# Kernel tuning notes

Measured on AMD Instinct MI355X. Metric: run time of the kernel, lower is better.

The kernel has to match this reference:

```python
import jax, jax.numpy as jnp
import numpy as np

B, T, V, H, E, MAX_OOV = 128, 200, 50257, 256, 128, 50


def setup_inputs() -> dict:
    key = jax.random.key(0)
    ks = jax.random.split(key, 17)
    s = 0.05  # param scale
    return {
        "decoder_input": jax.random.randint(ks[0], (B, 1), 0, V),
        "encoder_outputs": jax.random.normal(ks[1], (B, T, 2 * H), jnp.float32),
        "encoder_idxs": jax.random.randint(ks[2], (B, T), 0, V),
        "prev_state": jax.random.normal(ks[3], (1, B, H), jnp.float32),
        "selective_read": jax.random.normal(ks[4], (B, 1, 2 * H), jnp.float32) * s,
        "step": 1,
        "emb": jax.random.normal(ks[5], (V, E), jnp.float32) * s,
        "W_ih": jax.random.normal(ks[6], (3 * H, E + 2 * H), jnp.float32) * s,
        "W_hh": jax.random.normal(ks[7], (3 * H, H), jnp.float32) * s,
        "b_ih": jax.random.normal(ks[8], (3 * H,), jnp.float32) * s,
        "b_hh": jax.random.normal(ks[9], (3 * H,), jnp.float32) * s,
        "Wi_w": jax.random.normal(ks[10], (H, 2 * H), jnp.float32) * s,
        "Wi_b": jax.random.normal(ks[11], (H,), jnp.float32) * s,
        "Wg_w": jax.random.normal(ks[12], (V, H), jnp.float32) * s,
        "Wg_b": jax.random.normal(ks[13], (V,), jnp.float32) * s,
        "Wc_w": jax.random.normal(ks[14], (H, 2 * H), jnp.float32) * s,
        "Wc_b": jax.random.normal(ks[15], (H,), jnp.float32) * s,
    }


def _gru_cell(x, h, W_ih, W_hh, b_ih, b_hh):
    # torch GRUCell math, gate order r,z,n
    gi = x @ W_ih.T + b_ih
    gh = h @ W_hh.T + b_hh
    i_r, i_z, i_n = jnp.split(gi, 3, axis=-1)
    h_r, h_z, h_n = jnp.split(gh, 3, axis=-1)
    r = jax.nn.sigmoid(i_r + h_r)
    z = jax.nn.sigmoid(i_z + h_z)
    n = jnp.tanh(i_n + r * h_n)
    return (1.0 - z) * n + z * h


def reference(decoder_input, encoder_outputs, encoder_idxs, prev_state, selective_read,
              step, emb, W_ih, W_hh, b_ih, b_hh, Wi_w, Wi_b, Wg_w, Wg_b, Wc_w, Wc_b):
    dtype = encoder_outputs.dtype
    if step == 0:
        prev_state = (encoder_outputs[:, -1] @ Wi_w.T + Wi_b)[None]      # 1,B,H
        selective_read = jnp.zeros((B, 1, 2 * H), dtype)
    embedded = emb[decoder_input[:, 0]]                                   # B,E
    gru_in = jnp.concatenate([selective_read[:, 0], embedded], axis=-1)   # B,2H+E
    decode_hidden = _gru_cell(gru_in, prev_state[0], W_ih, W_hh, b_ih, b_hh)  # B,H

    score_g = decode_hidden @ Wg_w.T + Wg_b                               # B,V
    enc_proj = jnp.tanh(jnp.einsum('bte,he->bth', encoder_outputs, Wc_w) + Wc_b)  # B,T,H
    score_c = jnp.tanh(jnp.einsum('bth,bh->bt', enc_proj, decode_hidden))         # B,T
    score_c = score_c + jnp.where(encoder_idxs == 0, -10000.0, 0.0).astype(dtype)

    probs = jax.nn.softmax(jnp.concatenate([score_g, score_c], axis=1), axis=1)   # B,V+T
    prob_g, prob_c = probs[:, :V], probs[:, V:]
    prob_g = jnp.concatenate([prob_g, jnp.full((B, MAX_OOV), 1e-4, dtype)], axis=1)  # B,V+oov

    # copy-distribution aggregation: scatter-add prob_c by vocab id (replaces one-hot bmm)
    prob_c_to_g = jnp.zeros((B, V + MAX_OOV), dtype).at[
        jnp.arange(B)[:, None], encoder_idxs].add(prob_c)
    prob_out = (prob_c_to_g + prob_g)[:, None, :]                          # B,1,V+oov

    # selective read for next step
    match = (encoder_idxs == decoder_input).astype(dtype)                  # B,T
    tot = match.sum(axis=1, keepdims=True)
    match = jnp.where(tot > 1, match / tot, match)
    prob_appeared = prob_c * match
    selective_read_new = jnp.einsum('bt,bte->be', prob_appeared, encoder_outputs)[:, None, :]  # B,1,2H
    return prob_out, decode_hidden, selective_read_new
```

## Files before the change

kernel.cpp:

```cpp
#include <hip/hip_runtime.h>

typedef __bf16 bf16;
typedef __bf16 bf16x4 __attribute__((ext_vector_type(4)));
typedef __bf16 bf16x8 __attribute__((ext_vector_type(8)));
typedef float f32x4 __attribute__((ext_vector_type(4)));

#define B_ 128
#define T_ 200
#define V_ 50257
#define H_ 256
#define E_ 128
#define OOV_ 50
#define VO_ 50307
#define NRG 64
#define NTS 4
#define GSC 786
#define NROWP 50304
#define PSTR 800
#define PBSTR 50368
#define GPJ 400
#define GWPACK 12576

__device__ __forceinline__ float sigmoid_(float x) { return 1.0f / (1.0f + __expf(-x)); }
__device__ __forceinline__ float tanh_(float x) { return 1.0f - 2.0f / (__expf(2.0f * x) + 1.0f); }

__global__ void k_front(const float* Wc_w, bf16* WcPack,
                        const int* step_p, const float* enc, const float* prev,
                        const float* selread, const int* dec, const float* emb,
                        const float* Wi_w, const float* Wi_b,
                        float* hT, float* ginT,
                        const float* Wg_w, bf16* WgPack) {
    if (blockIdx.x < 128) {
        int gid = blockIdx.x * 256 + threadIdx.x;
        int n = gid >> 7;
        int k = (gid & 127) * 4;
        float4 v = *(const float4*)(Wc_w + n * 512 + k);
        int kstep = k >> 5, kin = k & 31;
        int q = kin >> 3, j0 = kin & 7;
        int r = n & 15, nt = n >> 4;
        int lane = q * 16 + r;
        bf16* d = WcPack + (((nt * 16 + kstep) * 64) + lane) * 8 + j0;
        d[0] = (bf16)v.x; d[1] = (bf16)v.y; d[2] = (bf16)v.z; d[3] = (bf16)v.w;
    } else if (blockIdx.x < 256) {
        int b = blockIdx.x - 128, t = threadIdx.x;
        int step = step_p[0];
        float h;
        if (step == 0) {
            float acc = Wi_b[t];
            const float* er = enc + (b * T_ + (T_ - 1)) * 512;
            const float* wr = Wi_w + t * 512;
            for (int k = 0; k < 512; ++k) acc += er[k] * wr[k];
            h = acc;
        } else {
            h = prev[b * H_ + t];
        }
        hT[t * B_ + b] = h;
        for (int k = t; k < 512; k += 256)
            ginT[k * B_ + b] = (step == 0) ? 0.0f : selread[b * 512 + k];
        if (t < E_)
            ginT[(512 + t) * B_ + b] = emb[dec[b] * E_ + t];
    } else {
        int gid = (blockIdx.x - 256) * 256 + threadIdx.x;
        int row = gid >> 6;
        int k = (gid & 63) * 4;
        float4 v = (row < V_) ? *(const float4*)(Wg_w + row * 256 + k)
                              : float4{0.f, 0.f, 0.f, 0.f};
        int nt = row >> 4, r = row & 15;
        int ks = k >> 5, kin = k & 31;
        int q = kin >> 3, j0 = kin & 7;
        int lane = q * 16 + r;
        bf16* d = WgPack + (((nt * 8 + ks) * 64) + lane) * 8 + j0;
        d[0] = (bf16)v.x; d[1] = (bf16)v.y; d[2] = (bf16)v.z; d[3] = (bf16)v.w;
    }
}

__global__ void k_gemm_gru(const float* W_ih, const float* b_ih,
                           const float* W_hh, const float* b_hh,
                           const float* ginT, const float* hT,
                           float* giT, float* ghT) {
    __shared__ float red[256];
    int rrow = blockIdx.x;
    int t = threadIdx.x;
    int b = t & 127, kh = t >> 7;
    const float* w = W_ih + rrow * 640 + kh * 320;
    const float* g = ginT + (kh * 320) * B_ + b;
    float a0 = 0.f, a1 = 0.f, a2 = 0.f, a3 = 0.f;
#pragma unroll 4
    for (int k = 0; k < 320; k += 4) {
        a0 += w[k]     * g[k * B_];
        a1 += w[k + 1] * g[(k + 1) * B_];
        a2 += w[k + 2] * g[(k + 2) * B_];
        a3 += w[k + 3] * g[(k + 3) * B_];
    }
    const float* w2 = W_hh + rrow * 256 + kh * 128;
    const float* hh = hT + (kh * 128) * B_ + b;
    float c0 = 0.f, c1 = 0.f, c2 = 0.f, c3 = 0.f;
#pragma unroll 4
    for (int k = 0; k < 128; k += 4) {
        c0 += w2[k]     * hh[k * B_];
        c1 += w2[k + 1] * hh[(k + 1) * B_];
        c2 += w2[k + 2] * hh[(k + 2) * B_];
        c3 += w2[k + 3] * hh[(k + 3) * B_];
    }
    red[t] = ((a0 + a1) + (a2 + a3));
    __syncthreads();
    if (kh == 0) giT[rrow * B_ + b] = b_ih[rrow] + red[b] + red[b + 128];
    __syncthreads();
    red[t] = ((c0 + c1) + (c2 + c3));
    __syncthreads();
    if (kh == 0) ghT[rrow * B_ + b] = b_hh[rrow] + red[b] + red[b + 128];
}

__global__ void k_gru_cell(const float* giT, const float* ghT, const float* hT,
                           float* out_dh, bf16* Apack) {
    int b = blockIdx.x, j = threadIdx.x;
    float ir = giT[j * B_ + b], iz = giT[(256 + j) * B_ + b], in_ = giT[(512 + j) * B_ + b];
    float hr = ghT[j * B_ + b], hz = ghT[(256 + j) * B_ + b], hn = ghT[(512 + j) * B_ + b];
    float hp = hT[j * B_ + b];
    float r = sigmoid_(ir + hr);
    float z = sigmoid_(iz + hz);
    float n = tanh_(in_ + r * hn);
    float h = (1.0f - z) * n + z * hp;
    out_dh[b * H_ + j] = h;
    int mt = b >> 4, rr = b & 15, ks = j >> 5, q = (j >> 3) & 3, jj = j & 7;
    Apack[(((mt * 8 + ks) * 64) + (q * 16 + rr)) * 8 + jj] = (bf16)h;
}

__global__ __launch_bounds__(512, 2) void k_score(const bf16* Apack, const bf16* WgPack,
                                                  const float* Wg_b,
                                                  bf16* expg, float* pg_part) {
    int tid = threadIdx.x;
    int w = tid >> 6, lane = tid & 63;
    int r = lane & 15, q = lane >> 4;
    int blk = blockIdx.x;
    int n0 = blk * NRG;
    const bf16* bbase = WgPack + (size_t)(blk * NTS * 8) * 512 + lane * 8;
    const bf16* abase = Apack + (w * 8) * 512 + lane * 8;
    f32x4 acc[NTS];
#pragma unroll
    for (int i = 0; i < NTS; ++i) acc[i] = (f32x4){0.f, 0.f, 0.f, 0.f};
#pragma unroll
    for (int ks = 0; ks < 8; ++ks) {
        bf16x8 a = *(const bf16x8*)(abase + ks * 512);
#pragma unroll
        for (int nt = 0; nt < NTS; ++nt) {
            bf16x8 bfr = *(const bf16x8*)(bbase + (nt * 8 + ks) * 512);
            acc[nt] = __builtin_amdgcn_mfma_f32_16x16x32_bf16(a, bfr, acc[nt], 0, 0, 0);
        }
    }
    float rsum[4] = {0.f, 0.f, 0.f, 0.f};
#pragma unroll
    for (int nt = 0; nt < NTS; ++nt) {
        int n = n0 + nt * 16 + r;
        bool valid = (n < V_);
        float wgb = Wg_b[valid ? n : (V_ - 1)];
#pragma unroll
        for (int rg = 0; rg < 4; ++rg) {
            int row = w * 16 + q * 4 + rg;
            float e = valid ? __expf(acc[nt][rg] + wgb) : 0.0f;
            rsum[rg] += e;
            expg[row * PBSTR + n] = (bf16)e;
        }
    }
#pragma unroll
    for (int rg = 0; rg < 4; ++rg) {
        float s = rsum[rg];
        s += __shfl_xor(s, 1);
        s += __shfl_xor(s, 2);
        s += __shfl_xor(s, 4);
        s += __shfl_xor(s, 8);
        if (r == 0) {
            int row = w * 16 + q * 4 + rg;
            pg_part[row * PSTR + blk] = s;
        }
    }
}

__global__ __launch_bounds__(256, 4) void k_proj(const float* enc, const bf16* WcPack,
                                                 const float* Wc_b, const float* dh,
                                                 const int* idxs, float* expc) {
    __shared__ unsigned char smem[34816];
    int tid = threadIdx.x;
    int w = tid >> 6, lane = tid & 63;
    int r = lane & 15, q = lane >> 4;
    int m0 = blockIdx.x * 64;
    bf16* As = (bf16*)smem;
    float* sred = (float*)(smem + 33792);
    f32x4 acc[16];
#pragma unroll
    for (int i = 0; i < 16; ++i) acc[i] = (f32x4){0.f, 0.f, 0.f, 0.f};
    for (int half = 0; half < 2; ++half) {
        __syncthreads();
#pragma unroll
        for (int ph = 0; ph < 2; ++ph) {
            float4 tmp[8];
#pragma unroll
            for (int j = 0; j < 8; ++j) {
                int f = (ph * 8 + j) * 256 + tid;
                int row = f >> 6, c4 = f & 63;
                tmp[j] = *(const float4*)(enc + (m0 + row) * 512 + half * 256 + c4 * 4);
            }
#pragma unroll
            for (int j = 0; j < 8; ++j) {
                int f = (ph * 8 + j) * 256 + tid;
                int row = f >> 6, c4 = f & 63;
                bf16x4 o;
                o[0] = (bf16)tmp[j].x; o[1] = (bf16)tmp[j].y;
                o[2] = (bf16)tmp[j].z; o[3] = (bf16)tmp[j].w;
                *(bf16x4*)(As + row * 264 + c4 * 4) = o;
            }
        }
        __syncthreads();
#pragma unroll
        for (int ks = 0; ks < 8; ++ks) {
            int kstep = half * 8 + ks;
            bf16x8 bfr[4];
#pragma unroll
            for (int ntl = 0; ntl < 4; ++ntl)
                bfr[ntl] = *(const bf16x8*)(WcPack + (((w * 4 + ntl) * 16 + kstep) * 64 + lane) * 8);
#pragma unroll
            for (int mt = 0; mt < 4; ++mt) {
                bf16x8 a = *(const bf16x8*)(As + (mt * 16 + r) * 264 + ks * 32 + q * 8);
#pragma unroll
                for (int ntl = 0; ntl < 4; ++ntl)
                    acc[mt * 4 + ntl] = __builtin_amdgcn_mfma_f32_16x16x32_bf16(a, bfr[ntl], acc[mt * 4 + ntl], 0, 0, 0);
            }
        }
    }
#pragma unroll
    for (int mt = 0; mt < 4; ++mt) {
#pragma unroll
        for (int rg = 0; rg < 4; ++rg) {
            int rowl = mt * 16 + q * 4 + rg;
            int row = m0 + rowl;
            int b = row / T_;
            float s = 0.0f;
#pragma unroll
            for (int ntl = 0; ntl < 4; ++ntl) {
                int n = (w * 4 + ntl) * 16 + r;
                float pv = tanh_(acc[mt * 4 + ntl][rg] + Wc_b[n]);
                s += pv * dh[b * H_ + n];
            }
            s += __shfl_xor(s, 1);
            s += __shfl_xor(s, 2);
            s += __shfl_xor(s, 4);
            s += __shfl_xor(s, 8);
            if (r == 0) sred[rowl * 4 + w] = s;
        }
    }
    __syncthreads();
    if (tid < 64) {
        float s = sred[tid * 4] + sred[tid * 4 + 1] + sred[tid * 4 + 2] + sred[tid * 4 + 3];
        int row = m0 + tid;
        int b = row / T_, t = row - b * T_;
        float sc = tanh_(s);
        if (idxs[b * T_ + t] == 0) sc -= 10000.0f;
        expc[row] = __expf(sc);
    }
}

__global__ void k_reduce(const float* pg_part, const float* expc_, const int* idxs,
                         const int* dec, const float* enc, float* inv_out,
                         float* out_sel) {
    __shared__ float red[256];
    __shared__ float cf[256];
    int b = blockIdx.x, t = threadIdx.x;
    float s = 0.0f;
    for (int i = t; i < GSC; i += 256) s += pg_part[b * PSTR + i];
    if (t < T_) s += expc_[b * T_ + t];
    red[t] = s;
    __syncthreads();
    for (int k = 128; k > 0; k >>= 1) {
        if (t < k) red[t] += red[t + k];
        __syncthreads();
    }
    float iv = 1.0f / red[0];
    if (t == 0) inv_out[b] = iv;
    __syncthreads();
    int d = dec[b];
    float ec = 0.0f;
    int m = 0;
    if (t < T_) {
        int ix = idxs[b * T_ + t];
        ec = expc_[b * T_ + t];
        m = (ix == d) ? 1 : 0;
    }
    cf[t] = m ? ec * iv : 0.0f;
    red[t] = m ? 1.0f : 0.0f;
    __syncthreads();
    for (int k = 128; k > 0; k >>= 1) {
        if (t < k) red[t] += red[t + k];
        __syncthreads();
    }
    float tot = red[0];
    float scale = (tot > 1.0f) ? 1.0f / tot : 1.0f;
    float a0 = 0.0f, a1 = 0.0f;
    for (int tt = 0; tt < T_; ++tt) {
        float c = cf[tt];
        if (c != 0.0f) {
            float wgt = c * scale;
            a0 += wgt * enc[(b * T_ + tt) * 512 + t];
            a1 += wgt * enc[(b * T_ + tt) * 512 + t + 256];
        }
    }
    out_sel[b * 512 + t] = a0;
    out_sel[b * 512 + t + 256] = a1;
}

__global__ __launch_bounds__(256) void k_normwrite(const bf16* expg, const float* inv,
                                                   float* out_prob) {
    int b = blockIdx.x >> 5, c = blockIdx.x & 31;
    int t = threadIdx.x;
    float iv = inv[b];
    int base = b * VO_;
    const bf16* eg = expg + b * PBSTR;
    int i4s = (base + 3) >> 2;
    int i4e = (base + VO_) >> 2;
    int head = (i4s << 2) - base;
    if (c == 0 && t < head) {
        int col = t;
        out_prob[base + col] = (float)eg[col] * iv;
    }
    int tail = (base + VO_) - (i4e << 2);
    if (c == 31 && t < tail) {
        int col = (i4e << 2) - base + t;
        out_prob[base + col] = (col < V_) ? (float)eg[col] * iv : 1e-4f;
    }
    int n4 = i4e - i4s;
    int per = (n4 + 31) >> 5;
    int s0 = i4s + c * per;
    int e0 = s0 + per; if (e0 > i4e) e0 = i4e;
    int sh = ((i4s << 2) - base) == 0 ? 0 : (4 - ((base) & 3)) & 3;
    sh = (4 - (base & 3)) & 3;
    for (int i4 = s0 + t; i4 < e0; i4 += 256) {
        int col = (i4 << 2) - base;
        int al = col & ~3;
        bf16x4 L0 = *(const bf16x4*)(eg + al);
        bf16x4 L1 = *(const bf16x4*)(eg + al + 4);
        float f0 = (float)L0[0], f1 = (float)L0[1], f2 = (float)L0[2], f3 = (float)L0[3];
        float f4 = (float)L1[0], f5 = (float)L1[1], f6 = (float)L1[2], f7 = (float)L1[3];
        float v0, v1, v2, v3;
        if (sh == 0)      { v0 = f0; v1 = f1; v2 = f2; v3 = f3; }
        else if (sh == 1) { v0 = f1; v1 = f2; v2 = f3; v3 = f4; }
        else if (sh == 2) { v0 = f2; v1 = f3; v2 = f4; v3 = f5; }
        else              { v0 = f3; v1 = f4; v2 = f5; v3 = f6; }
        float o0 = (col + 0 < V_) ? v0 * iv : 1e-4f;
        float o1 = (col + 1 < V_) ? v1 * iv : 1e-4f;
        float o2 = (col + 2 < V_) ? v2 * iv : 1e-4f;
        float o3 = (col + 3 < V_) ? v3 * iv : 1e-4f;
        *(float4*)(out_prob + (i4 << 2)) = make_float4(o0, o1, o2, o3);
    }
}

__global__ void k_scatter(const float* expc_, const int* idxs, const float* inv,
                          float* out_prob) {
    int b = blockIdx.x, t = threadIdx.x;
    if (t < T_) {
        int ix = idxs[b * T_ + t];
        atomicAdd(&out_prob[b * VO_ + ix], expc_[b * T_ + t] * inv[b]);
    }
}

extern "C" void kernel_launch(void* const* d_in, const int* in_sizes, int n_in,
                              void* d_out, int out_size, void* d_ws, size_t ws_size,
                              hipStream_t stream) {
    const int*   dec     = (const int*)d_in[0];
    const float* enc     = (const float*)d_in[1];
    const int*   idxs    = (const int*)d_in[2];
    const float* prev    = (const float*)d_in[3];
    const float* selread = (const float*)d_in[4];
    const int*   step_p  = (const int*)d_in[5];
    const float* emb     = (const float*)d_in[6];
    const float* W_ih    = (const float*)d_in[7];
    const float* W_hh    = (const float*)d_in[8];
    const float* b_ih    = (const float*)d_in[9];
    const float* b_hh    = (const float*)d_in[10];
    const float* Wi_w    = (const float*)d_in[11];
    const float* Wi_b    = (const float*)d_in[12];
    const float* Wg_w    = (const float*)d_in[13];
    const float* Wg_b    = (const float*)d_in[14];
    const float* Wc_w    = (const float*)d_in[15];
    const float* Wc_b    = (const float*)d_in[16];

    float* ws     = (float*)d_ws;
    float* hT     = ws;
    float* ginT   = ws + 32768;
    float* giT    = ws + 114688;
    float* ghT    = ws + 212992;
    float* inv    = ws + 311296;
    float* expc   = ws + 311552;
    float* pgp    = ws + 337152;
    bf16*  Apack  = (bf16*)(ws + 741376);
    bf16*  WcPack = (bf16*)(ws + 757760);
    bf16*  expg   = (bf16*)(ws + 823296);

    float* out      = (float*)d_out;
    float* out_prob = out;
    float* out_dh   = out + 6439296;
    float* out_sel  = out + 6439296 + 32768;
    bf16*  WgPack   = (bf16*)out;

    k_front<<<256 + GWPACK, 256, 0, stream>>>(Wc_w, WcPack, step_p, enc, prev, selread,
                                              dec, emb, Wi_w, Wi_b, hT, ginT,
                                              Wg_w, WgPack);
    k_gemm_gru<<<768, 256, 0, stream>>>(W_ih, b_ih, W_hh, b_hh, ginT, hT, giT, ghT);
    k_gru_cell<<<B_, 256, 0, stream>>>(giT, ghT, hT, out_dh, Apack);
    k_proj<<<GPJ, 256, 0, stream>>>(enc, WcPack, Wc_b, out_dh, idxs, expc);
    k_score<<<GSC, 512, 0, stream>>>(Apack, WgPack, Wg_b, expg, pgp);
    k_reduce<<<B_, 256, 0, stream>>>(pgp, expc, idxs, dec, enc, inv, out_sel);
    k_normwrite<<<B_ * 32, 256, 0, stream>>>(expg, inv, out_prob);
    k_scatter<<<B_, 256, 0, stream>>>(expc, idxs, inv, out_prob);
}
```

Before: 283.5 us.

## Pack Wg with 16-byte stores per thread and halve k_proj tile rows

The Wg_w to bf16 MFMA-layout packing now has each thread handle one row-fragment across all 8 k-steps and write whole bf16x8 vectors. This replaces 4 scalar bf16 stores per float4 and cuts the grid from 12576 to 786 blocks. Separately, k_proj now tiles 32 rows per block instead of 64, doubling the block count to 800 and halving LDS and accumulator use for better occupancy on a small GEMM. The trade-off is that the Wc fragment loads are amortized over fewer rows per block.

```diff
diff --git a/kernel.cpp b/kernel.cpp
--- a/kernel.cpp
+++ b/kernel.cpp
@@ -18,8 +18,7 @@
 #define NROWP 50304
 #define PSTR 800
 #define PBSTR 50368
-#define GPJ 400
-#define GWPACK 12576
+#define GPJ 800
 
 __device__ __forceinline__ float sigmoid_(float x) { return 1.0f / (1.0f + __expf(-x)); }
 __device__ __forceinline__ float tanh_(float x) { return 1.0f - 2.0f / (__expf(2.0f * x) + 1.0f); }
@@ -60,17 +59,28 @@
         if (t < E_)
             ginT[(512 + t) * B_ + b] = emb[dec[b] * E_ + t];
     } else {
-        int gid = (blockIdx.x - 256) * 256 + threadIdx.x;
-        int row = gid >> 6;
-        int k = (gid & 63) * 4;
-        float4 v = (row < V_) ? *(const float4*)(Wg_w + row * 256 + k)
-                              : float4{0.f, 0.f, 0.f, 0.f};
-        int nt = row >> 4, r = row & 15;
-        int ks = k >> 5, kin = k & 31;
-        int q = kin >> 3, j0 = kin & 7;
-        int lane = q * 16 + r;
-        bf16* d = WgPack + (((nt * 8 + ks) * 64) + lane) * 8 + j0;
-        d[0] = (bf16)v.x; d[1] = (bf16)v.y; d[2] = (bf16)v.z; d[3] = (bf16)v.w;
+        int pb = blockIdx.x - 256;
+        int t = threadIdx.x;
+        int w = t >> 6, lane = t & 63;
+        int r = lane & 15, q = lane >> 4;
+        int nt = pb * 4 + w;
+        int row = nt * 16 + r;
+        bool valid = (row < V_);
+        const float* src = Wg_w + (size_t)(valid ? row : (V_ - 1)) * 256 + q * 8;
+        bf16* dst = WgPack + ((size_t)(nt * 8) * 64 + lane) * 8;
+#pragma unroll
+        for (int ks = 0; ks < 8; ++ks) {
+            float4 va = *(const float4*)(src + ks * 32);
+            float4 vb = *(const float4*)(src + ks * 32 + 4);
+            bf16x8 o;
+            if (valid) {
+                o[0] = (bf16)va.x; o[1] = (bf16)va.y; o[2] = (bf16)va.z; o[3] = (bf16)va.w;
+                o[4] = (bf16)vb.x; o[5] = (bf16)vb.y; o[6] = (bf16)vb.z; o[7] = (bf16)vb.w;
+            } else {
+                o[0] = o[1] = o[2] = o[3] = o[4] = o[5] = o[6] = o[7] = (bf16)0.0f;
+            }
+            *(bf16x8*)(dst + (size_t)ks * 512) = o;
+        }
     }
 }
 
@@ -179,30 +189,30 @@
 __global__ __launch_bounds__(256, 4) void k_proj(const float* enc, const bf16* WcPack,
                                                  const float* Wc_b, const float* dh,
                                                  const int* idxs, float* expc) {
-    __shared__ unsigned char smem[34816];
+    __shared__ unsigned char smem[17408];
     int tid = threadIdx.x;
     int w = tid >> 6, lane = tid & 63;
     int r = lane & 15, q = lane >> 4;
-    int m0 = blockIdx.x * 64;
+    int m0 = blockIdx.x * 32;
     bf16* As = (bf16*)smem;
-    float* sred = (float*)(smem + 33792);
-    f32x4 acc[16];
-#pragma unroll
-    for (int i = 0; i < 16; ++i) acc[i] = (f32x4){0.f, 0.f, 0.f, 0.f};
+    float* sred = (float*)(smem + 16896);
+    f32x4 acc[8];
+#pragma unroll
+    for (int i = 0; i < 8; ++i) acc[i] = (f32x4){0.f, 0.f, 0.f, 0.f};
     for (int half = 0; half < 2; ++half) {
         __syncthreads();
 #pragma unroll
         for (int ph = 0; ph < 2; ++ph) {
-            float4 tmp[8];
-#pragma unroll
-            for (int j = 0; j < 8; ++j) {
-                int f = (ph * 8 + j) * 256 + tid;
+            float4 tmp[4];
+#pragma unroll
+            for (int j = 0; j < 4; ++j) {
+                int f = (ph * 4 + j) * 256 + tid;
                 int row = f >> 6, c4 = f & 63;
                 tmp[j] = *(const float4*)(enc + (m0 + row) * 512 + half * 256 + c4 * 4);
             }
 #pragma unroll
-            for (int j = 0; j < 8; ++j) {
-                int f = (ph * 8 + j) * 256 + tid;
+            for (int j = 0; j < 4; ++j) {
+                int f = (ph * 4 + j) * 256 + tid;
                 int row = f >> 6, c4 = f & 63;
                 bf16x4 o;
                 o[0] = (bf16)tmp[j].x; o[1] = (bf16)tmp[j].y;
@@ -219,7 +229,7 @@
             for (int ntl = 0; ntl < 4; ++ntl)
                 bfr[ntl] = *(const bf16x8*)(WcPack + (((w * 4 + ntl) * 16 + kstep) * 64 + lane) * 8);
 #pragma unroll
-            for (int mt = 0; mt < 4; ++mt) {
+            for (int mt = 0; mt < 2; ++mt) {
                 bf16x8 a = *(const bf16x8*)(As + (mt * 16 + r) * 264 + ks * 32 + q * 8);
 #pragma unroll
                 for (int ntl = 0; ntl < 4; ++ntl)
@@ -228,7 +238,7 @@
         }
     }
 #pragma unroll
-    for (int mt = 0; mt < 4; ++mt) {
+    for (int mt = 0; mt < 2; ++mt) {
 #pragma unroll
         for (int rg = 0; rg < 4; ++rg) {
             int rowl = mt * 16 + q * 4 + rg;
@@ -249,7 +259,7 @@
         }
     }
     __syncthreads();
-    if (tid < 64) {
+    if (tid < 32) {
         float s = sred[tid * 4] + sred[tid * 4 + 1] + sred[tid * 4 + 2] + sred[tid * 4 + 3];
         int row = m0 + tid;
         int b = row / T_, t = row - b * T_;
@@ -330,15 +340,14 @@
     int per = (n4 + 31) >> 5;
     int s0 = i4s + c * per;
     int e0 = s0 + per; if (e0 > i4e) e0 = i4e;
-    int sh = ((i4s << 2) - base) == 0 ? 0 : (4 - ((base) & 3)) & 3;
-    sh = (4 - (base & 3)) & 3;
+    int sh = (4 - (base & 3)) & 3;
     for (int i4 = s0 + t; i4 < e0; i4 += 256) {
         int col = (i4 << 2) - base;
         int al = col & ~3;
         bf16x4 L0 = *(const bf16x4*)(eg + al);
         bf16x4 L1 = *(const bf16x4*)(eg + al + 4);
         float f0 = (float)L0[0], f1 = (float)L0[1], f2 = (float)L0[2], f3 = (float)L0[3];
-        float f4 = (float)L1[0], f5 = (float)L1[1], f6 = (float)L1[2], f7 = (float)L1[3];
+        float f4 = (float)L1[0], f5 = (float)L1[1], f6 = (float)L1[2];
         float v0, v1, v2, v3;
         if (sh == 0)      { v0 = f0; v1 = f1; v2 = f2; v3 = f3; }
         else if (sh == 1) { v0 = f1; v1 = f2; v2 = f3; v3 = f4; }
@@ -400,9 +409,9 @@
     float* out_sel  = out + 6439296 + 32768;
     bf16*  WgPack   = (bf16*)out;
 
-    k_front<<<256 + GWPACK, 256, 0, stream>>>(Wc_w, WcPack, step_p, enc, prev, selread,
-                                              dec, emb, Wi_w, Wi_b, hT, ginT,
-                                              Wg_w, WgPack);
+    k_front<<<256 + GSC, 256, 0, stream>>>(Wc_w, WcPack, step_p, enc, prev, selread,
+                                           dec, emb, Wi_w, Wi_b, hT, ginT,
+                                           Wg_w, WgPack);
     k_gemm_gru<<<768, 256, 0, stream>>>(W_ih, b_ih, W_hh, b_hh, ginT, hT, giT, ghT);
     k_gru_cell<<<B_, 256, 0, stream>>>(giT, ghT, hT, out_dh, Apack);
     k_proj<<<GPJ, 256, 0, stream>>>(enc, WcPack, Wc_b, out_dh, idxs, expc);
```

Measured after the change: 271.1 us. 4.4% less time.
